# Performance work log

Hardware: AMD Instinct MI355X
Metric: run time of the kernel (lower is better)

## Reference

```python
import jax, jax.numpy as jnp
import numpy as np

B, DS, DM = 4, 64, 4096
NE, S = 1024, 2048


def setup_inputs() -> dict:
    key = jax.random.key(0)
    ks = jax.random.split(key, 9)
    std = 0.02
    return {
        "state": jax.random.normal(ks[0], (B, DS, DM), jnp.float32),
        "evicted_tokens": jax.random.normal(ks[1], (B, NE, DM), jnp.float32),
        "current_tokens": jax.random.normal(ks[2], (B, S, DM), jnp.float32),
        "W_key": std * jax.random.normal(ks[3], (DS, DM), jnp.float32),
        "W_beta_w": std * jax.random.normal(ks[4], (DS, DM), jnp.float32),
        "W_beta_b": jnp.zeros((DS,), jnp.float32),
        "W_query": std * jax.random.normal(ks[5], (DS, DM), jnp.float32),
        "gate_w": std * jax.random.normal(ks[6], (1, DM), jnp.float32),
        "gate_b": jnp.full((1,), -2.0, jnp.float32),  # gate_bias init
    }


def reference(state, evicted_tokens, current_tokens, W_key, W_beta_w, W_beta_b,
              W_query, gate_w, gate_b):
    # ---- compress: fold evicted tokens into SSM state ----
    # keys: [B, NE, DS]; softmax over the token axis (dim=1)
    keys = jnp.einsum('bnd,sd->bns', evicted_tokens, W_key)
    write_weights = jax.nn.softmax(keys, axis=1)
    # update: [B, DS, DM] = write_weights^T @ evicted_tokens
    update = jnp.einsum('bns,bnd->bsd', write_weights, evicted_tokens)
    summary = evicted_tokens.mean(axis=1)  # [B, DM]
    beta = jax.nn.sigmoid(summary @ W_beta_w.T + W_beta_b)  # [B, DS]
    new_state = beta[:, :, None] * state + update  # [B, DS, DM]
    # ---- query: gated linear-attention readout ----
    q = jnp.einsum('bld,sd->bls', current_tokens, W_query)  # [B, S, DS]
    retrieved = jnp.einsum('bls,bsd->bld', q, new_state)    # [B, S, DM]
    gate = jax.nn.sigmoid(current_tokens @ gate_w.T + gate_b)  # [B, S, 1]
    return gate * retrieved
```

## Files before the change

### kernel.cpp

```cpp
#include <hip/hip_runtime.h>

#define DM 4096
#define DSZ 64
#define NE 1024
#define SQ 2048
#define NB 4

typedef __attribute__((ext_vector_type(8))) short bf16x8;
typedef __attribute__((ext_vector_type(4))) float f32x4;

__device__ __forceinline__ unsigned f2bf(float f) {
  union { float f; unsigned u; } v; v.f = f;
  return (v.u + 0x7fffu + ((v.u >> 16) & 1u)) >> 16;
}
__device__ __forceinline__ unsigned pack2(float lo, float hi) {
  return f2bf(lo) | (f2bf(hi) << 16);
}

__launch_bounds__(256)
__global__ void k_keys(const float* __restrict__ ev, const float* __restrict__ Wk,
                       float* __restrict__ keys_part) {
  __shared__ __align__(16) unsigned short As[64][72];
  __shared__ __align__(16) unsigned short Bs[64][72];
  const int bid = blockIdx.x;
  const int ks = bid & 7, mt = (bid >> 3) & 15, b = bid >> 7;
  const int n0 = mt * 64;
  const int t = threadIdx.x;
  const int w = t >> 6, m15 = t & 15, quad = (t & 63) >> 4;
  const int rowS = t >> 2, seg = (t & 3) * 16;

  f32x4 acc[4];
#pragma unroll
  for (int i = 0; i < 4; ++i) acc[i] = (f32x4){0.f, 0.f, 0.f, 0.f};

  const float* ap = ev + ((size_t)(b * NE + n0 + rowS)) * DM + ks * 512 + seg;
  const float* bp = Wk + (size_t)rowS * DM + ks * 512 + seg;

  for (int ch = 0; ch < 8; ++ch) {
    float4 a0 = *(const float4*)(ap);
    float4 a1 = *(const float4*)(ap + 4);
    float4 a2 = *(const float4*)(ap + 8);
    float4 a3 = *(const float4*)(ap + 12);
    float4 b0 = *(const float4*)(bp);
    float4 b1 = *(const float4*)(bp + 4);
    float4 b2 = *(const float4*)(bp + 8);
    float4 b3 = *(const float4*)(bp + 12);
    uint4 pa0 = { pack2(a0.x,a0.y), pack2(a0.z,a0.w), pack2(a1.x,a1.y), pack2(a1.z,a1.w) };
    uint4 pa1 = { pack2(a2.x,a2.y), pack2(a2.z,a2.w), pack2(a3.x,a3.y), pack2(a3.z,a3.w) };
    uint4 pb0 = { pack2(b0.x,b0.y), pack2(b0.z,b0.w), pack2(b1.x,b1.y), pack2(b1.z,b1.w) };
    uint4 pb1 = { pack2(b2.x,b2.y), pack2(b2.z,b2.w), pack2(b3.x,b3.y), pack2(b3.z,b3.w) };
    *(uint4*)&As[rowS][seg]     = pa0;
    *(uint4*)&As[rowS][seg + 8] = pa1;
    *(uint4*)&Bs[rowS][seg]     = pb0;
    *(uint4*)&Bs[rowS][seg + 8] = pb1;
    __syncthreads();
#pragma unroll
    for (int kk = 0; kk < 2; ++kk) {
      bf16x8 af = *(const bf16x8*)&As[w * 16 + m15][kk * 32 + quad * 8];
#pragma unroll
      for (int tn = 0; tn < 4; ++tn) {
        bf16x8 bfr = *(const bf16x8*)&Bs[tn * 16 + m15][kk * 32 + quad * 8];
        acc[tn] = __builtin_amdgcn_mfma_f32_16x16x32_bf16(af, bfr, acc[tn], 0, 0, 0);
      }
    }
    __syncthreads();
    ap += 64; bp += 64;
  }
  const int n = n0 + w * 16 + quad * 4;
#pragma unroll
  for (int tn = 0; tn < 4; ++tn) {
    const int s = tn * 16 + m15;
    float4 v = { acc[tn][0], acc[tn][1], acc[tn][2], acc[tn][3] };
    *(float4*)&keys_part[(size_t)ks * (NB * DSZ * NE) + ((size_t)(b * DSZ + s)) * NE + n] = v;
  }
}

__launch_bounds__(256)
__global__ void k_sum(const float* __restrict__ ev, float* __restrict__ summary) {
  __shared__ float red[256];
  const int bid = blockIdx.x;
  const int b = bid >> 7, rem = bid & 127;
  const int d0 = (rem >> 1) * 64, half = rem & 1;
  const int t = threadIdx.x;
  const int dl = t & 63, g = t >> 6;
  float acc = 0.f;
  const float* p = ev + ((size_t)(b * NE + half * 512 + g * 128)) * DM + d0 + dl;
  for (int i = 0; i < 128; ++i) { acc += *p; p += DM; }
  red[t] = acc;
  __syncthreads();
  if (t < 64) {
    float tot = red[t] + red[t + 64] + red[t + 128] + red[t + 192];
    atomicAdd(&summary[b * DM + d0 + t], tot * (1.f / 1024.f));
  }
}

__launch_bounds__(256)
__global__ void k_beta(const float* __restrict__ summary, const float* __restrict__ Wbw,
                       const float* __restrict__ Wbb, float* __restrict__ beta) {
  __shared__ float red[256];
  const int b = blockIdx.x >> 6, s = blockIdx.x & 63;
  const int t = threadIdx.x;
  const float* sp = summary + b * DM + t * 16;
  const float* wp = Wbw + (size_t)s * DM + t * 16;
  float acc = 0.f;
#pragma unroll
  for (int j = 0; j < 4; ++j) {
    float4 a  = *(const float4*)(sp + j * 4);
    float4 w4 = *(const float4*)(wp + j * 4);
    acc += a.x * w4.x + a.y * w4.y + a.z * w4.z + a.w * w4.w;
  }
  red[t] = acc;
  __syncthreads();
  for (int off = 128; off > 0; off >>= 1) {
    if (t < off) red[t] += red[t + off];
    __syncthreads();
  }
  if (t == 0) {
    float x = red[0] + Wbb[s];
    beta[b * DSZ + s] = 1.f / (1.f + expf(-x));
  }
}

__launch_bounds__(256)
__global__ void k_softmax(const float* __restrict__ keys_part, unsigned short* __restrict__ ww_t) {
  __shared__ float red[256];
  const int b = blockIdx.x >> 6, s = blockIdx.x & 63;
  const int t = threadIdx.x;
  const size_t base = ((size_t)(b * DSZ + s)) * NE + t * 4;
  float4 k = {0.f, 0.f, 0.f, 0.f};
#pragma unroll
  for (int sl = 0; sl < 8; ++sl) {
    float4 p = *(const float4*)&keys_part[(size_t)sl * (NB * DSZ * NE) + base];
    k.x += p.x; k.y += p.y; k.z += p.z; k.w += p.w;
  }
  float m = fmaxf(fmaxf(k.x, k.y), fmaxf(k.z, k.w));
  red[t] = m;
  __syncthreads();
  for (int off = 128; off > 0; off >>= 1) {
    if (t < off) red[t] = fmaxf(red[t], red[t + off]);
    __syncthreads();
  }
  const float M = red[0];
  __syncthreads();
  float4 e = { expf(k.x - M), expf(k.y - M), expf(k.z - M), expf(k.w - M) };
  red[t] = e.x + e.y + e.z + e.w;
  __syncthreads();
  for (int off = 128; off > 0; off >>= 1) {
    if (t < off) red[t] += red[t + off];
    __syncthreads();
  }
  const float inv = 1.f / red[0];
  ushort4 o = { (unsigned short)f2bf(e.x * inv), (unsigned short)f2bf(e.y * inv),
                (unsigned short)f2bf(e.z * inv), (unsigned short)f2bf(e.w * inv) };
  *(ushort4*)&ww_t[((size_t)(b * DSZ + s)) * NE + t * 4] = o;
}

__launch_bounds__(256)
__global__ void k_update(const float* __restrict__ ev, const float* __restrict__ state,
                         const float* __restrict__ beta, const unsigned short* __restrict__ ww_t,
                         unsigned short* __restrict__ ns_t) {
  __shared__ __align__(16) unsigned short Aw[64][72];
  __shared__ __align__(16) unsigned short Bt[64][72];
  const int bid = blockIdx.x;
  const int dt = bid & 63, b = bid >> 6;
  const int d0 = dt * 64;
  const int t = threadIdx.x;
  const int w = t >> 6, m15 = t & 15, quad = (t & 63) >> 4;
  const int rowS = t >> 2, seg = (t & 3) * 16;
  const int npair = (t & 31) * 2, dseg = (t >> 5) * 8;

  f32x4 acc[4];
#pragma unroll
  for (int i = 0; i < 4; ++i) acc[i] = (f32x4){0.f, 0.f, 0.f, 0.f};

  for (int ch = 0; ch < 16; ++ch) {
    const int nch = ch * 64;
    const uint4* wsrc = (const uint4*)&ww_t[((size_t)(b * DSZ + rowS)) * NE + nch + seg];
    uint4 wa = wsrc[0], wb = wsrc[1];
    const float* e0 = ev + ((size_t)(b * NE + nch + npair)) * DM + d0 + dseg;
    const float* e1 = e0 + DM;
    float4 r00 = *(const float4*)(e0);
    float4 r01 = *(const float4*)(e0 + 4);
    float4 r10 = *(const float4*)(e1);
    float4 r11 = *(const float4*)(e1 + 4);
    *(uint4*)&Aw[rowS][seg]     = wa;
    *(uint4*)&Aw[rowS][seg + 8] = wb;
    *(unsigned*)&Bt[dseg + 0][npair] = pack2(r00.x, r10.x);
    *(unsigned*)&Bt[dseg + 1][npair] = pack2(r00.y, r10.y);
    *(unsigned*)&Bt[dseg + 2][npair] = pack2(r00.z, r10.z);
    *(unsigned*)&Bt[dseg + 3][npair] = pack2(r00.w, r10.w);
    *(unsigned*)&Bt[dseg + 4][npair] = pack2(r01.x, r11.x);
    *(unsigned*)&Bt[dseg + 5][npair] = pack2(r01.y, r11.y);
    *(unsigned*)&Bt[dseg + 6][npair] = pack2(r01.z, r11.z);
    *(unsigned*)&Bt[dseg + 7][npair] = pack2(r01.w, r11.w);
    __syncthreads();
#pragma unroll
    for (int kk = 0; kk < 2; ++kk) {
      bf16x8 af = *(const bf16x8*)&Aw[w * 16 + m15][kk * 32 + quad * 8];
#pragma unroll
      for (int tn = 0; tn < 4; ++tn) {
        bf16x8 bfr = *(const bf16x8*)&Bt[tn * 16 + m15][kk * 32 + quad * 8];
        acc[tn] = __builtin_amdgcn_mfma_f32_16x16x32_bf16(af, bfr, acc[tn], 0, 0, 0);
      }
    }
    __syncthreads();
  }
  const int sbase = w * 16 + quad * 4;
#pragma unroll
  for (int tn = 0; tn < 4; ++tn) {
    const int d = d0 + tn * 16 + m15;
    float v[4];
#pragma unroll
    for (int r = 0; r < 4; ++r) {
      const int s = sbase + r;
      v[r] = beta[b * DSZ + s] * state[((size_t)(b * DSZ + s)) * DM + d] + acc[tn][r];
    }
    ushort4 o = { (unsigned short)f2bf(v[0]), (unsigned short)f2bf(v[1]),
                  (unsigned short)f2bf(v[2]), (unsigned short)f2bf(v[3]) };
    *(ushort4*)&ns_t[((size_t)(b * DM + d)) * DSZ + sbase] = o;
  }
}

__launch_bounds__(256)
__global__ void k_q(const float* __restrict__ cur, const float* __restrict__ Wq,
                    const float* __restrict__ gate_w,
                    float* __restrict__ q_part, float* __restrict__ gate_acc) {
  __shared__ __align__(16) unsigned short As[64][72];
  __shared__ __align__(16) unsigned short Bs[64][72];
  __shared__ float gw[64];
  __shared__ float gred[256];
  const int bid = blockIdx.x;
  const int ks = bid & 3, mt = (bid >> 2) & 31, b = bid >> 7;
  const int l0 = mt * 64;
  const int t = threadIdx.x;
  const int w = t >> 6, m15 = t & 15, quad = (t & 63) >> 4;
  const int rowS = t >> 2, seg = (t & 3) * 16;

  f32x4 acc[4];
#pragma unroll
  for (int i = 0; i < 4; ++i) acc[i] = (f32x4){0.f, 0.f, 0.f, 0.f};
  float gpart = 0.f;

  const float* ap = cur + ((size_t)(b * SQ + l0 + rowS)) * DM + ks * 1024 + seg;
  const float* bp = Wq + (size_t)rowS * DM + ks * 1024 + seg;
  const float* gp = gate_w + ks * 1024;

  for (int ch = 0; ch < 16; ++ch) {
    float4 a0 = *(const float4*)(ap);
    float4 a1 = *(const float4*)(ap + 4);
    float4 a2 = *(const float4*)(ap + 8);
    float4 a3 = *(const float4*)(ap + 12);
    float4 b0 = *(const float4*)(bp);
    float4 b1 = *(const float4*)(bp + 4);
    float4 b2 = *(const float4*)(bp + 8);
    float4 b3 = *(const float4*)(bp + 12);
    if (t < 16) *(float4*)&gw[t * 4] = *(const float4*)(gp + ch * 64 + t * 4);
    uint4 pa0 = { pack2(a0.x,a0.y), pack2(a0.z,a0.w), pack2(a1.x,a1.y), pack2(a1.z,a1.w) };
    uint4 pa1 = { pack2(a2.x,a2.y), pack2(a2.z,a2.w), pack2(a3.x,a3.y), pack2(a3.z,a3.w) };
    uint4 pb0 = { pack2(b0.x,b0.y), pack2(b0.z,b0.w), pack2(b1.x,b1.y), pack2(b1.z,b1.w) };
    uint4 pb1 = { pack2(b2.x,b2.y), pack2(b2.z,b2.w), pack2(b3.x,b3.y), pack2(b3.z,b3.w) };
    *(uint4*)&As[rowS][seg]     = pa0;
    *(uint4*)&As[rowS][seg + 8] = pa1;
    *(uint4*)&Bs[rowS][seg]     = pb0;
    *(uint4*)&Bs[rowS][seg + 8] = pb1;
    __syncthreads();
    {
      const float* g = &gw[seg];
      gpart += a0.x*g[0]  + a0.y*g[1]  + a0.z*g[2]  + a0.w*g[3]
             + a1.x*g[4]  + a1.y*g[5]  + a1.z*g[6]  + a1.w*g[7]
             + a2.x*g[8]  + a2.y*g[9]  + a2.z*g[10] + a2.w*g[11]
             + a3.x*g[12] + a3.y*g[13] + a3.z*g[14] + a3.w*g[15];
    }
#pragma unroll
    for (int kk = 0; kk < 2; ++kk) {
      bf16x8 af = *(const bf16x8*)&As[w * 16 + m15][kk * 32 + quad * 8];
#pragma unroll
      for (int tn = 0; tn < 4; ++tn) {
        bf16x8 bfr = *(const bf16x8*)&Bs[tn * 16 + m15][kk * 32 + quad * 8];
        acc[tn] = __builtin_amdgcn_mfma_f32_16x16x32_bf16(af, bfr, acc[tn], 0, 0, 0);
      }
    }
    __syncthreads();
    ap += 64; bp += 64;
  }
  const int lrow = l0 + w * 16 + quad * 4;
#pragma unroll
  for (int tn = 0; tn < 4; ++tn) {
#pragma unroll
    for (int r = 0; r < 4; ++r) {
      q_part[(size_t)ks * (NB * SQ * DSZ) + ((size_t)(b * SQ + lrow + r)) * DSZ + tn * 16 + m15] =
          acc[tn][r];
    }
  }
  gred[t] = gpart;
  __syncthreads();
  if (t < 64) {
    float tot = gred[4 * t] + gred[4 * t + 1] + gred[4 * t + 2] + gred[4 * t + 3];
    atomicAdd(&gate_acc[b * SQ + l0 + t], tot);
  }
}

__launch_bounds__(256)
__global__ void k_qcvt(const float* __restrict__ q_part, unsigned short* __restrict__ qbf) {
  const int i = (blockIdx.x * 256 + threadIdx.x) * 4;
  const int SL = NB * SQ * DSZ;
  float4 v0 = *(const float4*)&q_part[i];
  float4 v1 = *(const float4*)&q_part[i + SL];
  float4 v2 = *(const float4*)&q_part[i + 2 * SL];
  float4 v3 = *(const float4*)&q_part[i + 3 * SL];
  float x = v0.x + v1.x + v2.x + v3.x;
  float y = v0.y + v1.y + v2.y + v3.y;
  float z = v0.z + v1.z + v2.z + v3.z;
  float u = v0.w + v1.w + v2.w + v3.w;
  ushort4 o = { (unsigned short)f2bf(x), (unsigned short)f2bf(y),
                (unsigned short)f2bf(z), (unsigned short)f2bf(u) };
  *(ushort4*)&qbf[i] = o;
}

__launch_bounds__(256)
__global__ void k_out(const unsigned short* __restrict__ qbf, const unsigned short* __restrict__ ns_t,
                      const float* __restrict__ gate_acc, const float* __restrict__ gate_b,
                      float* __restrict__ out) {
  const int bid = blockIdx.x;
  const int dt = bid & 63, lt = (bid >> 6) & 31, b = bid >> 11;
  const int d0 = dt * 64, l0 = lt * 64;
  const int t = threadIdx.x;
  const int w = t >> 6, m15 = t & 15, quad = (t & 63) >> 4;
  const int la = l0 + w * 16 + m15;
  f32x4 acc[4];
#pragma unroll
  for (int i = 0; i < 4; ++i) acc[i] = (f32x4){0.f, 0.f, 0.f, 0.f};
#pragma unroll
  for (int kk = 0; kk < 2; ++kk) {
    bf16x8 af = *(const bf16x8*)&qbf[((size_t)(b * SQ + la)) * DSZ + kk * 32 + quad * 8];
#pragma unroll
    for (int tn = 0; tn < 4; ++tn) {
      const int d = d0 + tn * 16 + m15;
      bf16x8 bfr = *(const bf16x8*)&ns_t[((size_t)(b * DM + d)) * DSZ + kk * 32 + quad * 8];
      acc[tn] = __builtin_amdgcn_mfma_f32_16x16x32_bf16(af, bfr, acc[tn], 0, 0, 0);
    }
  }
  const float gb = gate_b[0];
  const int lbase = l0 + w * 16 + quad * 4;
  float g[4];
#pragma unroll
  for (int r = 0; r < 4; ++r)
    g[r] = 1.f / (1.f + expf(-(gate_acc[b * SQ + lbase + r] + gb)));
#pragma unroll
  for (int tn = 0; tn < 4; ++tn) {
    const int d = d0 + tn * 16 + m15;
#pragma unroll
    for (int r = 0; r < 4; ++r)
      out[((size_t)(b * SQ + lbase + r)) * DM + d] = g[r] * acc[tn][r];
  }
}

extern "C" void kernel_launch(void* const* d_in, const int* in_sizes, int n_in,
                              void* d_out, int out_size, void* d_ws, size_t ws_size,
                              hipStream_t stream) {
  const float* state   = (const float*)d_in[0];
  const float* evicted = (const float*)d_in[1];
  const float* current = (const float*)d_in[2];
  const float* Wkey    = (const float*)d_in[3];
  const float* Wbw     = (const float*)d_in[4];
  const float* Wbb     = (const float*)d_in[5];
  const float* Wq      = (const float*)d_in[6];
  const float* gate_w  = (const float*)d_in[7];
  const float* gate_b  = (const float*)d_in[8];
  float* out = (float*)d_out;

  float* f = (float*)d_ws;
  float* keys_part = f;
  float* q_part    = keys_part + 8 * 262144;
  float* summary   = q_part + 4 * 524288;
  float* gate_acc  = summary + 16384;
  float* beta      = gate_acc + 8192;
  unsigned short* ww_t = (unsigned short*)(beta + 256);
  unsigned short* qbf  = ww_t + 262144;
  unsigned short* ns_t = qbf + 524288;

  hipMemsetAsync(summary, 0, (16384 + 8192) * sizeof(float), stream);

  k_keys   <<<512,  256, 0, stream>>>(evicted, Wkey, keys_part);
  k_sum    <<<512,  256, 0, stream>>>(evicted, summary);
  k_beta   <<<256,  256, 0, stream>>>(summary, Wbw, Wbb, beta);
  k_softmax<<<256,  256, 0, stream>>>(keys_part, ww_t);
  k_update <<<256,  256, 0, stream>>>(evicted, state, beta, ww_t, ns_t);
  k_q      <<<512,  256, 0, stream>>>(current, Wq, gate_w, q_part, gate_acc);
  k_qcvt   <<<512,  256, 0, stream>>>(q_part, qbf);
  k_out    <<<8192, 256, 0, stream>>>(qbf, ns_t, gate_acc, gate_b, out);
}
```

Measured before the change: 396.9 us.

## Double-buffer LDS and prefetch global tiles in GEMM kernels, use wave-shuffle reductions

The keys, update and query GEMM kernels now use two LDS buffers and load the next chunk from global memory into registers while MFMAs run on the current one. This removes the second barrier per iteration and hides load latency. k_update is split into 32-column tiles with 512 blocks to give more parallelism. k_q stages all gate weights for its slice once at the start instead of once per chunk. The beta and softmax reductions switch from LDS trees to wave shuffles plus a small cross-wave step. The cost is roughly double the LDS footprint and extra registers held across the loop, which may lower occupancy.

After: 386.0 us. -2.7%, faster.

```diff
diff --git a/kernel.cpp b/kernel.cpp
--- a/kernel.cpp
+++ b/kernel.cpp
@@ -17,11 +17,20 @@
   return f2bf(lo) | (f2bf(hi) << 16);
 }
 
+__device__ __forceinline__ void load8(const float* __restrict__ ap, const float* __restrict__ bp,
+                                      float4& a0, float4& a1, float4& a2, float4& a3,
+                                      float4& b0, float4& b1, float4& b2, float4& b3) {
+  a0 = *(const float4*)(ap);      a1 = *(const float4*)(ap + 4);
+  a2 = *(const float4*)(ap + 8);  a3 = *(const float4*)(ap + 12);
+  b0 = *(const float4*)(bp);      b1 = *(const float4*)(bp + 4);
+  b2 = *(const float4*)(bp + 8);  b3 = *(const float4*)(bp + 12);
+}
+
 __launch_bounds__(256)
 __global__ void k_keys(const float* __restrict__ ev, const float* __restrict__ Wk,
                        float* __restrict__ keys_part) {
-  __shared__ __align__(16) unsigned short As[64][72];
-  __shared__ __align__(16) unsigned short Bs[64][72];
+  __shared__ __align__(16) unsigned short As[2][64][72];
+  __shared__ __align__(16) unsigned short Bs[2][64][72];
   const int bid = blockIdx.x;
   const int ks = bid & 7, mt = (bid >> 3) & 15, b = bid >> 7;
   const int n0 = mt * 64;
@@ -36,35 +45,29 @@
   const float* ap = ev + ((size_t)(b * NE + n0 + rowS)) * DM + ks * 512 + seg;
   const float* bp = Wk + (size_t)rowS * DM + ks * 512 + seg;
 
+  float4 a0, a1, a2, a3, b0, b1, b2, b3;
+  load8(ap, bp, a0, a1, a2, a3, b0, b1, b2, b3);
+  int cur = 0;
   for (int ch = 0; ch < 8; ++ch) {
-    float4 a0 = *(const float4*)(ap);
-    float4 a1 = *(const float4*)(ap + 4);
-    float4 a2 = *(const float4*)(ap + 8);
-    float4 a3 = *(const float4*)(ap + 12);
-    float4 b0 = *(const float4*)(bp);
-    float4 b1 = *(const float4*)(bp + 4);
-    float4 b2 = *(const float4*)(bp + 8);
-    float4 b3 = *(const float4*)(bp + 12);
-    uint4 pa0 = { pack2(a0.x,a0.y), pack2(a0.z,a0.w), pack2(a1.x,a1.y), pack2(a1.z,a1.w) };
-    uint4 pa1 = { pack2(a2.x,a2.y), pack2(a2.z,a2.w), pack2(a3.x,a3.y), pack2(a3.z,a3.w) };
-    uint4 pb0 = { pack2(b0.x,b0.y), pack2(b0.z,b0.w), pack2(b1.x,b1.y), pack2(b1.z,b1.w) };
-    uint4 pb1 = { pack2(b2.x,b2.y), pack2(b2.z,b2.w), pack2(b3.x,b3.y), pack2(b3.z,b3.w) };
-    *(uint4*)&As[rowS][seg]     = pa0;
-    *(uint4*)&As[rowS][seg + 8] = pa1;
-    *(uint4*)&Bs[rowS][seg]     = pb0;
-    *(uint4*)&Bs[rowS][seg + 8] = pb1;
+    *(uint4*)&As[cur][rowS][seg]     = (uint4){ pack2(a0.x,a0.y), pack2(a0.z,a0.w), pack2(a1.x,a1.y), pack2(a1.z,a1.w) };
+    *(uint4*)&As[cur][rowS][seg + 8] = (uint4){ pack2(a2.x,a2.y), pack2(a2.z,a2.w), pack2(a3.x,a3.y), pack2(a3.z,a3.w) };
+    *(uint4*)&Bs[cur][rowS][seg]     = (uint4){ pack2(b0.x,b0.y), pack2(b0.z,b0.w), pack2(b1.x,b1.y), pack2(b1.z,b1.w) };
+    *(uint4*)&Bs[cur][rowS][seg + 8] = (uint4){ pack2(b2.x,b2.y), pack2(b2.z,b2.w), pack2(b3.x,b3.y), pack2(b3.z,b3.w) };
     __syncthreads();
+    if (ch < 7) {
+      ap += 64; bp += 64;
+      load8(ap, bp, a0, a1, a2, a3, b0, b1, b2, b3);
+    }
 #pragma unroll
     for (int kk = 0; kk < 2; ++kk) {
-      bf16x8 af = *(const bf16x8*)&As[w * 16 + m15][kk * 32 + quad * 8];
+      bf16x8 af = *(const bf16x8*)&As[cur][w * 16 + m15][kk * 32 + quad * 8];
 #pragma unroll
       for (int tn = 0; tn < 4; ++tn) {
-        bf16x8 bfr = *(const bf16x8*)&Bs[tn * 16 + m15][kk * 32 + quad * 8];
+        bf16x8 bfr = *(const bf16x8*)&Bs[cur][tn * 16 + m15][kk * 32 + quad * 8];
         acc[tn] = __builtin_amdgcn_mfma_f32_16x16x32_bf16(af, bfr, acc[tn], 0, 0, 0);
       }
     }
-    __syncthreads();
-    ap += 64; bp += 64;
+    cur ^= 1;
   }
   const int n = n0 + w * 16 + quad * 4;
 #pragma unroll
@@ -97,7 +100,7 @@
 __launch_bounds__(256)
 __global__ void k_beta(const float* __restrict__ summary, const float* __restrict__ Wbw,
                        const float* __restrict__ Wbb, float* __restrict__ beta) {
-  __shared__ float red[256];
+  __shared__ float wred[4];
   const int b = blockIdx.x >> 6, s = blockIdx.x & 63;
   const int t = threadIdx.x;
   const float* sp = summary + b * DM + t * 16;
@@ -109,21 +112,19 @@
     float4 w4 = *(const float4*)(wp + j * 4);
     acc += a.x * w4.x + a.y * w4.y + a.z * w4.z + a.w * w4.w;
   }
-  red[t] = acc;
-  __syncthreads();
-  for (int off = 128; off > 0; off >>= 1) {
-    if (t < off) red[t] += red[t + off];
-    __syncthreads();
-  }
+#pragma unroll
+  for (int off = 32; off > 0; off >>= 1) acc += __shfl_xor(acc, off);
+  if ((t & 63) == 0) wred[t >> 6] = acc;
+  __syncthreads();
   if (t == 0) {
-    float x = red[0] + Wbb[s];
+    float x = wred[0] + wred[1] + wred[2] + wred[3] + Wbb[s];
     beta[b * DSZ + s] = 1.f / (1.f + expf(-x));
   }
 }
 
 __launch_bounds__(256)
 __global__ void k_softmax(const float* __restrict__ keys_part, unsigned short* __restrict__ ww_t) {
-  __shared__ float red[256];
+  __shared__ float wred[8];
   const int b = blockIdx.x >> 6, s = blockIdx.x & 63;
   const int t = threadIdx.x;
   const size_t base = ((size_t)(b * DSZ + s)) * NE + t * 4;
@@ -134,22 +135,18 @@
     k.x += p.x; k.y += p.y; k.z += p.z; k.w += p.w;
   }
   float m = fmaxf(fmaxf(k.x, k.y), fmaxf(k.z, k.w));
-  red[t] = m;
-  __syncthreads();
-  for (int off = 128; off > 0; off >>= 1) {
-    if (t < off) red[t] = fmaxf(red[t], red[t + off]);
-    __syncthreads();
-  }
-  const float M = red[0];
-  __syncthreads();
+#pragma unroll
+  for (int off = 32; off > 0; off >>= 1) m = fmaxf(m, __shfl_xor(m, off));
+  if ((t & 63) == 0) wred[t >> 6] = m;
+  __syncthreads();
+  const float M = fmaxf(fmaxf(wred[0], wred[1]), fmaxf(wred[2], wred[3]));
   float4 e = { expf(k.x - M), expf(k.y - M), expf(k.z - M), expf(k.w - M) };
-  red[t] = e.x + e.y + e.z + e.w;
-  __syncthreads();
-  for (int off = 128; off > 0; off >>= 1) {
-    if (t < off) red[t] += red[t + off];
-    __syncthreads();
-  }
-  const float inv = 1.f / red[0];
+  float ss = e.x + e.y + e.z + e.w;
+#pragma unroll
+  for (int off = 32; off > 0; off >>= 1) ss += __shfl_xor(ss, off);
+  if ((t & 63) == 0) wred[4 + (t >> 6)] = ss;
+  __syncthreads();
+  const float inv = 1.f / (wred[4] + wred[5] + wred[6] + wred[7]);
   ushort4 o = { (unsigned short)f2bf(e.x * inv), (unsigned short)f2bf(e.y * inv),
                 (unsigned short)f2bf(e.z * inv), (unsigned short)f2bf(e.w * inv) };
   *(ushort4*)&ww_t[((size_t)(b * DSZ + s)) * NE + t * 4] = o;
@@ -159,55 +156,53 @@
 __global__ void k_update(const float* __restrict__ ev, const float* __restrict__ state,
                          const float* __restrict__ beta, const unsigned short* __restrict__ ww_t,
                          unsigned short* __restrict__ ns_t) {
-  __shared__ __align__(16) unsigned short Aw[64][72];
-  __shared__ __align__(16) unsigned short Bt[64][72];
-  const int bid = blockIdx.x;
-  const int dt = bid & 63, b = bid >> 6;
-  const int d0 = dt * 64;
+  __shared__ __align__(16) unsigned short Aw[2][64][72];
+  __shared__ __align__(16) unsigned short Bt[2][32][72];
+  const int bid = blockIdx.x;
+  const int dt = bid & 127, b = bid >> 7;
+  const int d0 = dt * 32;
   const int t = threadIdx.x;
   const int w = t >> 6, m15 = t & 15, quad = (t & 63) >> 4;
   const int rowS = t >> 2, seg = (t & 3) * 16;
-  const int npair = (t & 31) * 2, dseg = (t >> 5) * 8;
-
-  f32x4 acc[4];
-#pragma unroll
-  for (int i = 0; i < 4; ++i) acc[i] = (f32x4){0.f, 0.f, 0.f, 0.f};
-
+  const int npair = (t & 31) * 2, dquad = (t >> 5) * 4;
+
+  f32x4 acc[2];
+#pragma unroll
+  for (int i = 0; i < 2; ++i) acc[i] = (f32x4){0.f, 0.f, 0.f, 0.f};
+
+  const unsigned short* wp = ww_t + ((size_t)(b * DSZ + rowS)) * NE + seg;
+  const float* ep = ev + ((size_t)(b * NE + npair)) * DM + d0 + dquad;
+
+  uint4 wa = *(const uint4*)(wp), wb = *(const uint4*)(wp + 8);
+  float4 r0 = *(const float4*)(ep), r1 = *(const float4*)(ep + DM);
+  int cur = 0;
   for (int ch = 0; ch < 16; ++ch) {
-    const int nch = ch * 64;
-    const uint4* wsrc = (const uint4*)&ww_t[((size_t)(b * DSZ + rowS)) * NE + nch + seg];
-    uint4 wa = wsrc[0], wb = wsrc[1];
-    const float* e0 = ev + ((size_t)(b * NE + nch + npair)) * DM + d0 + dseg;
-    const float* e1 = e0 + DM;
-    float4 r00 = *(const float4*)(e0);
-    float4 r01 = *(const float4*)(e0 + 4);
-    float4 r10 = *(const float4*)(e1);
-    float4 r11 = *(const float4*)(e1 + 4);
-    *(uint4*)&Aw[rowS][seg]     = wa;
-    *(uint4*)&Aw[rowS][seg + 8] = wb;
-    *(unsigned*)&Bt[dseg + 0][npair] = pack2(r00.x, r10.x);
-    *(unsigned*)&Bt[dseg + 1][npair] = pack2(r00.y, r10.y);
-    *(unsigned*)&Bt[dseg + 2][npair] = pack2(r00.z, r10.z);
-    *(unsigned*)&Bt[dseg + 3][npair] = pack2(r00.w, r10.w);
-    *(unsigned*)&Bt[dseg + 4][npair] = pack2(r01.x, r11.x);
-    *(unsigned*)&Bt[dseg + 5][npair] = pack2(r01.y, r11.y);
-    *(unsigned*)&Bt[dseg + 6][npair] = pack2(r01.z, r11.z);
-    *(unsigned*)&Bt[dseg + 7][npair] = pack2(r01.w, r11.w);
+    *(uint4*)&Aw[cur][rowS][seg]     = wa;
+    *(uint4*)&Aw[cur][rowS][seg + 8] = wb;
+    *(unsigned*)&Bt[cur][dquad + 0][npair] = pack2(r0.x, r1.x);
+    *(unsigned*)&Bt[cur][dquad + 1][npair] = pack2(r0.y, r1.y);
+    *(unsigned*)&Bt[cur][dquad + 2][npair] = pack2(r0.z, r1.z);
+    *(unsigned*)&Bt[cur][dquad + 3][npair] = pack2(r0.w, r1.w);
     __syncthreads();
+    if (ch < 15) {
+      wp += 64; ep += (size_t)64 * DM;
+      wa = *(const uint4*)(wp); wb = *(const uint4*)(wp + 8);
+      r0 = *(const float4*)(ep); r1 = *(const float4*)(ep + DM);
+    }
 #pragma unroll
     for (int kk = 0; kk < 2; ++kk) {
-      bf16x8 af = *(const bf16x8*)&Aw[w * 16 + m15][kk * 32 + quad * 8];
-#pragma unroll
-      for (int tn = 0; tn < 4; ++tn) {
-        bf16x8 bfr = *(const bf16x8*)&Bt[tn * 16 + m15][kk * 32 + quad * 8];
+      bf16x8 af = *(const bf16x8*)&Aw[cur][w * 16 + m15][kk * 32 + quad * 8];
+#pragma unroll
+      for (int tn = 0; tn < 2; ++tn) {
+        bf16x8 bfr = *(const bf16x8*)&Bt[cur][tn * 16 + m15][kk * 32 + quad * 8];
         acc[tn] = __builtin_amdgcn_mfma_f32_16x16x32_bf16(af, bfr, acc[tn], 0, 0, 0);
       }
     }
-    __syncthreads();
+    cur ^= 1;
   }
   const int sbase = w * 16 + quad * 4;
 #pragma unroll
-  for (int tn = 0; tn < 4; ++tn) {
+  for (int tn = 0; tn < 2; ++tn) {
     const int d = d0 + tn * 16 + m15;
     float v[4];
 #pragma unroll
@@ -222,12 +217,12 @@
 }
 
 __launch_bounds__(256)
-__global__ void k_q(const float* __restrict__ cur, const float* __restrict__ Wq,
+__global__ void k_q(const float* __restrict__ cur_, const float* __restrict__ Wq,
                     const float* __restrict__ gate_w,
                     float* __restrict__ q_part, float* __restrict__ gate_acc) {
-  __shared__ __align__(16) unsigned short As[64][72];
-  __shared__ __align__(16) unsigned short Bs[64][72];
-  __shared__ float gw[64];
+  __shared__ __align__(16) unsigned short As[2][64][72];
+  __shared__ __align__(16) unsigned short Bs[2][64][72];
+  __shared__ float gwAll[1024];
   __shared__ float gred[256];
   const int bid = blockIdx.x;
   const int ks = bid & 3, mt = (bid >> 2) & 31, b = bid >> 7;
@@ -241,47 +236,41 @@
   for (int i = 0; i < 4; ++i) acc[i] = (f32x4){0.f, 0.f, 0.f, 0.f};
   float gpart = 0.f;
 
-  const float* ap = cur + ((size_t)(b * SQ + l0 + rowS)) * DM + ks * 1024 + seg;
+  *(float4*)&gwAll[t * 4] = *(const float4*)(gate_w + ks * 1024 + t * 4);
+
+  const float* ap = cur_ + ((size_t)(b * SQ + l0 + rowS)) * DM + ks * 1024 + seg;
   const float* bp = Wq + (size_t)rowS * DM + ks * 1024 + seg;
-  const float* gp = gate_w + ks * 1024;
-
+
+  float4 a0, a1, a2, a3, b0, b1, b2, b3;
+  load8(ap, bp, a0, a1, a2, a3, b0, b1, b2, b3);
+  int cur = 0;
   for (int ch = 0; ch < 16; ++ch) {
-    float4 a0 = *(const float4*)(ap);
-    float4 a1 = *(const float4*)(ap + 4);
-    float4 a2 = *(const float4*)(ap + 8);
-    float4 a3 = *(const float4*)(ap + 12);
-    float4 b0 = *(const float4*)(bp);
-    float4 b1 = *(const float4*)(bp + 4);
-    float4 b2 = *(const float4*)(bp + 8);
-    float4 b3 = *(const float4*)(bp + 12);
-    if (t < 16) *(float4*)&gw[t * 4] = *(const float4*)(gp + ch * 64 + t * 4);
-    uint4 pa0 = { pack2(a0.x,a0.y), pack2(a0.z,a0.w), pack2(a1.x,a1.y), pack2(a1.z,a1.w) };
-    uint4 pa1 = { pack2(a2.x,a2.y), pack2(a2.z,a2.w), pack2(a3.x,a3.y), pack2(a3.z,a3.w) };
-    uint4 pb0 = { pack2(b0.x,b0.y), pack2(b0.z,b0.w), pack2(b1.x,b1.y), pack2(b1.z,b1.w) };
-    uint4 pb1 = { pack2(b2.x,b2.y), pack2(b2.z,b2.w), pack2(b3.x,b3.y), pack2(b3.z,b3.w) };
-    *(uint4*)&As[rowS][seg]     = pa0;
-    *(uint4*)&As[rowS][seg + 8] = pa1;
-    *(uint4*)&Bs[rowS][seg]     = pb0;
-    *(uint4*)&Bs[rowS][seg + 8] = pb1;
+    *(uint4*)&As[cur][rowS][seg]     = (uint4){ pack2(a0.x,a0.y), pack2(a0.z,a0.w), pack2(a1.x,a1.y), pack2(a1.z,a1.w) };
+    *(uint4*)&As[cur][rowS][seg + 8] = (uint4){ pack2(a2.x,a2.y), pack2(a2.z,a2.w), pack2(a3.x,a3.y), pack2(a3.z,a3.w) };
+    *(uint4*)&Bs[cur][rowS][seg]     = (uint4){ pack2(b0.x,b0.y), pack2(b0.z,b0.w), pack2(b1.x,b1.y), pack2(b1.z,b1.w) };
+    *(uint4*)&Bs[cur][rowS][seg + 8] = (uint4){ pack2(b2.x,b2.y), pack2(b2.z,b2.w), pack2(b3.x,b3.y), pack2(b3.z,b3.w) };
     __syncthreads();
     {
-      const float* g = &gw[seg];
+      const float* g = &gwAll[ch * 64 + seg];
       gpart += a0.x*g[0]  + a0.y*g[1]  + a0.z*g[2]  + a0.w*g[3]
              + a1.x*g[4]  + a1.y*g[5]  + a1.z*g[6]  + a1.w*g[7]
              + a2.x*g[8]  + a2.y*g[9]  + a2.z*g[10] + a2.w*g[11]
              + a3.x*g[12] + a3.y*g[13] + a3.z*g[14] + a3.w*g[15];
     }
+    if (ch < 15) {
+      ap += 64; bp += 64;
+      load8(ap, bp, a0, a1, a2, a3, b0, b1, b2, b3);
+    }
 #pragma unroll
     for (int kk = 0; kk < 2; ++kk) {
-      bf16x8 af = *(const bf16x8*)&As[w * 16 + m15][kk * 32 + quad * 8];
+      bf16x8 af = *(const bf16x8*)&As[cur][w * 16 + m15][kk * 32 + quad * 8];
 #pragma unroll
       for (int tn = 0; tn < 4; ++tn) {
-        bf16x8 bfr = *(const bf16x8*)&Bs[tn * 16 + m15][kk * 32 + quad * 8];
+        bf16x8 bfr = *(const bf16x8*)&Bs[cur][tn * 16 + m15][kk * 32 + quad * 8];
         acc[tn] = __builtin_amdgcn_mfma_f32_16x16x32_bf16(af, bfr, acc[tn], 0, 0, 0);
       }
     }
-    __syncthreads();
-    ap += 64; bp += 64;
+    cur ^= 1;
   }
   const int lrow = l0 + w * 16 + quad * 4;
 #pragma unroll
@@ -385,7 +374,7 @@
   k_sum    <<<512,  256, 0, stream>>>(evicted, summary);
   k_beta   <<<256,  256, 0, stream>>>(summary, Wbw, Wbb, beta);
   k_softmax<<<256,  256, 0, stream>>>(keys_part, ww_t);
-  k_update <<<256,  256, 0, stream>>>(evicted, state, beta, ww_t, ns_t);
+  k_update <<<512,  256, 0, stream>>>(evicted, state, beta, ww_t, ns_t);
   k_q      <<<512,  256, 0, stream>>>(current, Wq, gate_w, q_part, gate_acc);
   k_qcvt   <<<512,  256, 0, stream>>>(q_part, qbf);
   k_out    <<<8192, 256, 0, stream>>>(qbf, ns_t, gate_acc, gate_b, out);
```
